# Kernel tuning notes

Hardware: AMD Instinct MI355X
Metric: run time of the kernel (lower is better)

The kernel has to match this reference:

```python
import jax, jax.numpy as jnp
import numpy as np

B, I, H = 8192, 1024, 1024

def _xavier(key, out_f, in_f):
    limit = (6.0 / (in_f + out_f)) ** 0.5
    return jax.random.uniform(key, (out_f, in_f), jnp.float32, -limit, limit)

def setup_inputs() -> dict:
    key = jax.random.key(0)
    ks = jax.random.split(key, 11)
    inp = {
        'x': jax.random.normal(ks[0], (B, I), jnp.float32),
        'h': jax.random.normal(ks[1], (B, H), jnp.float32),
        'c': jax.random.normal(ks[2], (B, H), jnp.float32),
    }
    names = ['Wxi', 'Whi', 'Wxf', 'Whf', 'Wxo', 'Who', 'Wxg', 'Whg']
    for n, k in zip(names, ks[3:]):
        in_f = I if n[1] == 'x' else H
        inp[n + '_w'] = _xavier(k, H, in_f)
        inp[n + '_b'] = jnp.zeros((H,), jnp.float32)
    return inp

def reference(x, h, c,
              Wxi_w, Wxi_b, Whi_w, Whi_b,
              Wxf_w, Wxf_b, Whf_w, Whf_b,
              Wxo_w, Wxo_b, Who_w, Who_b,
              Wxg_w, Wxg_b, Whg_w, Whg_b):
    Wx = jnp.concatenate([Wxi_w, Wxf_w, Wxo_w, Wxg_w], axis=0)  # [4H, I]
    Wh = jnp.concatenate([Whi_w, Whf_w, Who_w, Whg_w], axis=0)  # [4H, H]
    bx = jnp.concatenate([Wxi_b, Wxf_b, Wxo_b, Wxg_b], axis=0)  # [4H]
    bh = jnp.concatenate([Whi_b, Whf_b, Who_b, Whg_b], axis=0)  # [4H]
    z = x @ Wx.T + bx + h @ Wh.T + bh  # [B, 4H]
    zi, zf, zo, zg = jnp.split(z, 4, axis=-1)
    it = jax.nn.sigmoid(zi)
    ft = jax.nn.sigmoid(zf)
    ot = jax.nn.sigmoid(zo)
    gt = jnp.tanh(zg)
    c_next = ft * c + it * gt
    h_next = ot * jnp.tanh(c_next)
    return (h_next, c_next)
```

## Files before the change

### kernel.cpp

```cpp
#include <hip/hip_runtime.h>
#include <hip/hip_bf16.h>
#include <cstdint>


typedef __bf16 bf16;
typedef __attribute__((ext_vector_type(8))) bf16 bf16x8;
typedef __attribute__((ext_vector_type(4))) float f32x4;

#define CN_OFF 8388608

__device__ __forceinline__ void gload16(const bf16* g, bf16* l) {
  __builtin_amdgcn_global_load_lds(
      (const __attribute__((address_space(1))) void*)g,
      (__attribute__((address_space(3))) void*)l, 16, 0, 0);
}

__device__ __forceinline__ bf16x8 cvt8(f32x4 v0, f32x4 v1) {
  bf16x8 o;
  o[0]=(bf16)v0[0]; o[1]=(bf16)v0[1]; o[2]=(bf16)v0[2]; o[3]=(bf16)v0[3];
  o[4]=(bf16)v1[0]; o[5]=(bf16)v1[1]; o[6]=(bf16)v1[2]; o[7]=(bf16)v1[3];
  return o;
}

__global__ __launch_bounds__(256) void pack_all(
    const float* __restrict__ x, const float* __restrict__ h,
    const float* __restrict__ wxi, const float* __restrict__ whi,
    const float* __restrict__ wxf, const float* __restrict__ whf,
    const float* __restrict__ wxo, const float* __restrict__ who,
    const float* __restrict__ wxg, const float* __restrict__ whg,
    const float* __restrict__ bxi, const float* __restrict__ bhi,
    const float* __restrict__ bxf, const float* __restrict__ bhf,
    const float* __restrict__ bxo, const float* __restrict__ bho,
    const float* __restrict__ bxg, const float* __restrict__ bhg,
    bf16* __restrict__ A2, bf16* __restrict__ B2, float* __restrict__ Bcomb) {
  __shared__ __align__(16) bf16 lds[8192];
  const int t = threadIdx.x;
  const int bid = blockIdx.x;

  if (bid < 2048) {
    const int mb = bid >> 5;
    const int wm = (bid >> 4) & 1;
    const int q  = bid & 15;
    const int rowbase = mb * 128 + wm * 64;
    const float* srcM; int k0;
    if (q < 8) { srcM = x; k0 = q * 128; } else { srcM = h; k0 = q * 128 - 1024; }
#pragma unroll
    for (int r = 0; r < 4; ++r) {
      const int rl = r * 16 + (t >> 4);
      const int cc = (t & 15) * 8;
      const float* s = srcM + (size_t)(rowbase + rl) * 1024 + k0 + cc;
      f32x4 v0 = *(const f32x4*)s;
      f32x4 v1 = *(const f32x4*)(s + 4);
      const int chunkS = (t & 15) ^ (rl & 7);
      *(bf16x8*)((char*)lds + rl * 256 + chunkS * 16) = cvt8(v0, v1);
    }
    __syncthreads();
#pragma unroll
    for (int r = 0; r < 4; ++r) {
      const int idx = r * 256 + t;
      const int fj  = idx >> 6;
      const int ktL = fj >> 2, mi = fj & 3;
      const int l   = idx & 63;
      const int srow = mi * 16 + (l & 15);
      const int chunkS = (ktL * 4 + (l >> 4)) ^ (srow & 7);
      bf16x8 o = *(const bf16x8*)((const char*)lds + srow * 256 + chunkS * 16);
      size_t el = ((size_t)mb * 64 + q * 4 + ktL) * 4096 + (size_t)wm * 2048 + mi * 512 + l * 8;
      *(bf16x8*)(A2 + el) = o;
    }
  } else {
    const int bid2 = bid - 2048;
    const int nb   = bid2 >> 6;
    const int gate = (bid2 >> 4) & 3;
    const int q    = bid2 & 15;
    const float* wxm = (gate == 0) ? wxi : (gate == 1) ? wxf : (gate == 2) ? wxo : wxg;
    const float* whm = (gate == 0) ? whi : (gate == 1) ? whf : (gate == 2) ? who : whg;
    const float* srcM; int k0;
    if (q < 8) { srcM = wxm; k0 = q * 128; } else { srcM = whm; k0 = q * 128 - 1024; }
    const int jbase = nb * 32;
#pragma unroll
    for (int r = 0; r < 2; ++r) {
      const int rl = r * 16 + (t >> 4);
      const int cc = (t & 15) * 8;
      const float* s = srcM + (size_t)(jbase + rl) * 1024 + k0 + cc;
      f32x4 v0 = *(const f32x4*)s;
      f32x4 v1 = *(const f32x4*)(s + 4);
      const int chunkS = (t & 15) ^ (rl & 7);
      *(bf16x8*)((char*)lds + rl * 256 + chunkS * 16) = cvt8(v0, v1);
    }
    __syncthreads();
#pragma unroll
    for (int r = 0; r < 2; ++r) {
      const int idx = r * 256 + t;
      const int fj  = idx >> 6;
      const int ktL = fj >> 1, wn = fj & 1;
      const int l   = idx & 63;
      const int srow = wn * 16 + (l & 15);
      const int chunkS = (ktL * 4 + (l >> 4)) ^ (srow & 7);
      bf16x8 o = *(const bf16x8*)((const char*)lds + srow * 256 + chunkS * 16);
      size_t el = ((size_t)nb * 64 + q * 4 + ktL) * 4096 + (size_t)wn * 2048 + gate * 512 + l * 8;
      *(bf16x8*)(B2 + el) = o;
    }
    if (q == 0 && t < 32) {
      const float* bxv = (gate == 0) ? bxi : (gate == 1) ? bxf : (gate == 2) ? bxo : bxg;
      const float* bhv = (gate == 0) ? bhi : (gate == 1) ? bhf : (gate == 2) ? bho : bhg;
      const int wn = t >> 4, jl = t & 15;
      const int j = nb * 32 + wn * 16 + jl;
      Bcomb[(nb * 2 + wn) * 64 + gate * 16 + jl] = bxv[j] + bhv[j];
    }
  }
}

__device__ __forceinline__ float sigf(float v) { return 1.f / (1.f + __expf(-v)); }
__device__ __forceinline__ float tanhfast(float v) {
  v = fminf(15.f, fmaxf(-15.f, v));
  float e = __expf(2.f * v);
  return (e - 1.f) / (e + 1.f);
}

__global__ __launch_bounds__(512, 2) void gemm_lstm(const bf16* __restrict__ A2,
                                                    const bf16* __restrict__ B2,
                                                    const float* __restrict__ Bcomb,
                                                    const float* __restrict__ c,
                                                    float* __restrict__ out) {
  __shared__ __align__(16) bf16 lds[65536];
  const int t    = threadIdx.x;
  const int wave = t >> 6;
  const int lane = t & 63;

  const int bid = blockIdx.x;
  const int xcd = bid & 7;
  const int idx = bid >> 3;
  const int bn  = xcd * 2 + (idx & 1);
  const int bm  = idx >> 1;

  const int wr  = wave >> 2;
  const int wc  = wave & 3;
  const int nbL = wc >> 1, wn = wc & 1;
  const int lrow = lane & 15, lkg = lane >> 4;

  const int tEl = t * 8;
  const int wEl = (t & ~63) * 8;

  const bf16* aSrc0 = A2 + (size_t)(2 * bm)     * 64 * 4096;
  const bf16* aSrc1 = A2 + (size_t)(2 * bm + 1) * 64 * 4096;
  const bf16* bSrc0 = B2 + (size_t)(2 * bn)     * 64 * 4096;
  const bf16* bSrc1 = B2 + (size_t)(2 * bn + 1) * 64 * 4096;

  auto stage = [&](int tile, int buf) {
    const size_t kOff = (size_t)tile * 8192;
    bf16* d = lds + buf * 32768;
    const bf16* s0 = aSrc0 + kOff;
    const bf16* s1 = aSrc1 + kOff;
    const bf16* s2 = bSrc0 + kOff;
    const bf16* s3 = bSrc1 + kOff;
#pragma unroll
    for (int hh = 0; hh < 2; ++hh) {
      gload16(s0 + hh * 4096 + tEl, d +         hh * 4096 + wEl);
      gload16(s1 + hh * 4096 + tEl, d +  8192 + hh * 4096 + wEl);
      gload16(s2 + hh * 4096 + tEl, d + 16384 + hh * 4096 + wEl);
      gload16(s3 + hh * 4096 + tEl, d + 24576 + hh * 4096 + wEl);
    }
  };

  f32x4 acc[8][4] = {};

  stage(0, 0);
  __syncthreads();

  for (int kt2 = 0; kt2 < 32; ++kt2) {
    const int p = kt2 & 1;
    if (kt2 + 1 < 32) stage(kt2 + 1, p ^ 1);
    const bf16* bufA = lds + p * 32768 + wr * 8192;
    const bf16* bufB = lds + p * 32768 + 16384 + nbL * 8192 + wn * 2048;
#pragma unroll
    for (int ktL = 0; ktL < 2; ++ktL) {
      bf16x8 af[8], bfr[4];
#pragma unroll
      for (int i = 0; i < 8; ++i)
        af[i] = *(const bf16x8*)(bufA + ktL * 4096 + i * 512 + lane * 8);
#pragma unroll
      for (int g = 0; g < 4; ++g)
        bfr[g] = *(const bf16x8*)(bufB + ktL * 4096 + g * 512 + lane * 8);
      __builtin_amdgcn_s_setprio(1);
#pragma unroll
      for (int i = 0; i < 8; ++i)
#pragma unroll
        for (int g = 0; g < 4; ++g)
          acc[i][g] = __builtin_amdgcn_mfma_f32_16x16x32_bf16(af[i], bfr[g], acc[i][g], 0, 0, 0);
      __builtin_amdgcn_s_setprio(0);
    }
    __syncthreads();
  }

  const int nb = bn * 2 + nbL;
  const int jg = (nb * 2 + wn) * 16 + lrow;
  const int bbase = (nb * 2 + wn) * 64 + lrow;
  const float bi  = Bcomb[bbase +  0];
  const float bf_ = Bcomb[bbase + 16];
  const float bo  = Bcomb[bbase + 32];
  const float bg  = Bcomb[bbase + 48];

#pragma unroll
  for (int i = 0; i < 8; ++i) {
    const int row0 = (2 * bm + wr) * 128 + (i >> 2) * 64 + (i & 3) * 16 + lkg * 4;
    float cv[4];
#pragma unroll
    for (int r = 0; r < 4; ++r)
      cv[r] = c[(size_t)(row0 + r) * 1024 + jg];
#pragma unroll
    for (int r = 0; r < 4; ++r) {
      float zi = acc[i][0][r] + bi;
      float zf = acc[i][1][r] + bf_;
      float zo = acc[i][2][r] + bo;
      float zg = acc[i][3][r] + bg;
      float it = sigf(zi), ft = sigf(zf), ot = sigf(zo), gt = tanhfast(zg);
      float cn = ft * cv[r] + it * gt;
      size_t off = (size_t)(row0 + r) * 1024 + jg;
      out[off] = ot * tanhfast(cn);
      out[CN_OFF + off] = cn;
    }
  }
}

extern "C" void kernel_launch(void* const* d_in, const int* in_sizes, int n_in,
                              void* d_out, int out_size, void* d_ws, size_t ws_size,
                              hipStream_t stream) {
  const float* x   = (const float*)d_in[0];
  const float* h   = (const float*)d_in[1];
  const float* c   = (const float*)d_in[2];
  const float* Wxi = (const float*)d_in[3];  const float* bxi = (const float*)d_in[4];
  const float* Whi = (const float*)d_in[5];  const float* bhi = (const float*)d_in[6];
  const float* Wxf = (const float*)d_in[7];  const float* bxf = (const float*)d_in[8];
  const float* Whf = (const float*)d_in[9];  const float* bhf = (const float*)d_in[10];
  const float* Wxo = (const float*)d_in[11]; const float* bxo = (const float*)d_in[12];
  const float* Who = (const float*)d_in[13]; const float* bho = (const float*)d_in[14];
  const float* Wxg = (const float*)d_in[15]; const float* bxg = (const float*)d_in[16];
  const float* Whg = (const float*)d_in[17]; const float* bhg = (const float*)d_in[18];
  float* out = (float*)d_out;

  bf16*  Abuf  = (bf16*)d_ws;
  bf16*  Wbuf  = Abuf + (size_t)8192 * 2048;
  float* Bcomb = (float*)(Wbuf + (size_t)4096 * 2048);

  pack_all<<<4096, 256, 0, stream>>>(x, h,
                                     Wxi, Whi, Wxf, Whf, Wxo, Who, Wxg, Whg,
                                     bxi, bhi, bxf, bhf, bxo, bho, bxg, bhg,
                                     Abuf, Wbuf, Bcomb);
  gemm_lstm<<<512, 512, 0, stream>>>(Abuf, Wbuf, Bcomb, c, out);
}
```

Baseline: 316.9 us.

## Switch GEMM mainloop to 4-buffer LDS ring with prefetch depth two

The K loop now stages half-size K tiles, with one tile per iteration instead of two. They go into a four-slot LDS ring and are prefetched two tiles ahead. The two __syncthreads per iteration are replaced by an explicit vmcnt wait plus a single s_barrier. The goal is to overlap global-to-LDS loads with MFMA work and cut barrier cost. In exchange the loop runs twice as many iterations and relies on hand-tuned waitcnt values being correct.

```diff
diff --git a/kernel.cpp b/kernel.cpp
--- a/kernel.cpp
+++ b/kernel.cpp
@@ -147,49 +147,43 @@
   const bf16* bSrc1 = B2 + (size_t)(2 * bn + 1) * 64 * 4096;
 
   auto stage = [&](int tile, int buf) {
-    const size_t kOff = (size_t)tile * 8192;
-    bf16* d = lds + buf * 32768;
-    const bf16* s0 = aSrc0 + kOff;
-    const bf16* s1 = aSrc1 + kOff;
-    const bf16* s2 = bSrc0 + kOff;
-    const bf16* s3 = bSrc1 + kOff;
-#pragma unroll
-    for (int hh = 0; hh < 2; ++hh) {
-      gload16(s0 + hh * 4096 + tEl, d +         hh * 4096 + wEl);
-      gload16(s1 + hh * 4096 + tEl, d +  8192 + hh * 4096 + wEl);
-      gload16(s2 + hh * 4096 + tEl, d + 16384 + hh * 4096 + wEl);
-      gload16(s3 + hh * 4096 + tEl, d + 24576 + hh * 4096 + wEl);
-    }
+    const size_t kOff = (size_t)tile * 4096;
+    bf16* d = lds + buf * 16384;
+    gload16(aSrc0 + kOff + tEl, d +         wEl);
+    gload16(aSrc1 + kOff + tEl, d +  4096 + wEl);
+    gload16(bSrc0 + kOff + tEl, d +  8192 + wEl);
+    gload16(bSrc1 + kOff + tEl, d + 12288 + wEl);
   };
 
   f32x4 acc[8][4] = {};
 
   stage(0, 0);
-  __syncthreads();
-
-  for (int kt2 = 0; kt2 < 32; ++kt2) {
-    const int p = kt2 & 1;
-    if (kt2 + 1 < 32) stage(kt2 + 1, p ^ 1);
-    const bf16* bufA = lds + p * 32768 + wr * 8192;
-    const bf16* bufB = lds + p * 32768 + 16384 + nbL * 8192 + wn * 2048;
-#pragma unroll
-    for (int ktL = 0; ktL < 2; ++ktL) {
-      bf16x8 af[8], bfr[4];
-#pragma unroll
-      for (int i = 0; i < 8; ++i)
-        af[i] = *(const bf16x8*)(bufA + ktL * 4096 + i * 512 + lane * 8);
+  stage(1, 1);
+
+  for (int kt = 0; kt < 64; ++kt) {
+    const int p = kt & 3;
+    if (kt < 63) asm volatile("s_waitcnt vmcnt(4)" ::: "memory");
+    else         asm volatile("s_waitcnt vmcnt(0)" ::: "memory");
+    __builtin_amdgcn_s_barrier();
+    asm volatile("" ::: "memory");
+    if (kt + 2 < 64) stage(kt + 2, (kt + 2) & 3);
+
+    const bf16* bufA = lds + p * 16384 + wr * 4096;
+    const bf16* bufB = lds + p * 16384 + 8192 + nbL * 4096 + wn * 2048;
+    bf16x8 af[8], bfr[4];
+#pragma unroll
+    for (int i = 0; i < 8; ++i)
+      af[i] = *(const bf16x8*)(bufA + i * 512 + lane * 8);
+#pragma unroll
+    for (int g = 0; g < 4; ++g)
+      bfr[g] = *(const bf16x8*)(bufB + g * 512 + lane * 8);
+    __builtin_amdgcn_s_setprio(1);
+#pragma unroll
+    for (int i = 0; i < 8; ++i)
 #pragma unroll
       for (int g = 0; g < 4; ++g)
-        bfr[g] = *(const bf16x8*)(bufB + ktL * 4096 + g * 512 + lane * 8);
-      __builtin_amdgcn_s_setprio(1);
-#pragma unroll
-      for (int i = 0; i < 8; ++i)
-#pragma unroll
-        for (int g = 0; g < 4; ++g)
-          acc[i][g] = __builtin_amdgcn_mfma_f32_16x16x32_bf16(af[i], bfr[g], acc[i][g], 0, 0, 0);
-      __builtin_amdgcn_s_setprio(0);
-    }
-    __syncthreads();
+        acc[i][g] = __builtin_amdgcn_mfma_f32_16x16x32_bf16(af[i], bfr[g], acc[i][g], 0, 0, 0);
+    __builtin_amdgcn_s_setprio(0);
   }
 
   const int nb = bn * 2 + nbL;
```

Measured after the change: 319.1 us. About the same (+0.7%).
